# Kernel optimization log

Measured on AMD Instinct MI355X. Metric: run time of the kernel, lower is better.

The kernel has to match this reference:

```python
import jax, jax.numpy as jnp
import numpy as np

N_NODES = 100000   # multiple of 20 (tile factor)
N_BASE = N_NODES // 20
N_EDGES = 3200000  # avg degree 32


def setup_inputs() -> dict:
    key = jax.random.key(0)
    ks = jax.random.split(key, 12)
    x1 = jax.random.normal(ks[0], (N_NODES, 15), dtype=jnp.float32)
    x2 = jax.random.normal(ks[1], (N_BASE, 4), dtype=jnp.float32)
    edges = jax.random.randint(ks[2], (2, N_EDGES), 0, N_NODES, dtype=jnp.int64)
    # params (PyTorch Linear convention: y = x @ W.T + b)
    W1 = jax.random.normal(ks[3], (15, 15), dtype=jnp.float32) * 0.1
    b1 = jax.random.normal(ks[4], (15,), dtype=jnp.float32) * 0.1
    Wg = jax.random.normal(ks[5], (15, 34), dtype=jnp.float32) * 0.1  # GCNConv weight
    bg = jax.random.normal(ks[6], (15,), dtype=jnp.float32) * 0.1
    W3 = jax.random.normal(ks[7], (1, 34), dtype=jnp.float32) * 0.1
    b3 = jax.random.normal(ks[8], (1,), dtype=jnp.float32) * 0.1
    W4 = jax.random.normal(ks[9], (19, 19), dtype=jnp.float32) * 0.1
    b4 = jax.random.normal(ks[10], (19,), dtype=jnp.float32) * 0.1
    return {"x1": x1, "x2": x2, "edges": edges, "W1": W1, "b1": b1,
            "Wg": Wg, "bg": bg, "W3": W3, "b3": b3, "W4": W4, "b4": b4}


def reference(x1, x2, edges, W1, b1, Wg, bg, W3, b3, W4, b4):
    N = x1.shape[0]
    # b = layer4(cat([x1, tile(x2, (20,1))]))
    x2t = jnp.tile(x2, (20, 1))                       # [N, 4]
    b = jnp.concatenate([x1, x2t], axis=1) @ W4.T + b4  # [N, 19]
    a = jax.nn.relu(x1 @ W1.T + b1)                     # [N, 15]

    # GCN normalization with self-loops (PyG GCNConv defaults)
    row = jnp.concatenate([edges[0], jnp.arange(N, dtype=edges.dtype)])
    col = jnp.concatenate([edges[1], jnp.arange(N, dtype=edges.dtype)])
    deg = jax.ops.segment_sum(jnp.ones_like(col, dtype=x1.dtype), col, num_segments=N)
    dinv = jnp.where(deg > 0, deg ** -0.5, 0.0)
    norm = dinv[row] * dinv[col]                       # [E+N]

    for _ in range(5):
        h = jnp.concatenate([a, b], axis=1) @ Wg.T     # [N, 15]
        agg = jax.ops.segment_sum(h[row] * norm[:, None], col, num_segments=N)
        a = jax.nn.relu(agg + bg)

    out = jnp.concatenate([a, b], axis=1) @ W3.T + b3  # [N, 1]
    return jnp.tanh(out.mean())
```

## Files before the change

kernel.cpp:

```cpp
#include <hip/hip_runtime.h>
#include <hip/hip_fp16.h>
#include <math.h>

#define N_NODES 100000
#define N_BASE  5000
#define N_EDGES 3200000
#define NBKT    391
#define CAPB    9472
#define EPB     4096
#define GEB     782

__device__ inline unsigned pkh(float a, float b) {
    return (unsigned)__half_as_ushort(__float2half_rn(a)) |
           ((unsigned)__half_as_ushort(__float2half_rn(b)) << 16);
}

__device__ inline unsigned hadd2u(unsigned a, unsigned b) {
    __half2 r = __hadd2(*(__half2*)&a, *(__half2*)&b);
    return *(unsigned*)&r;
}

__global__ __launch_bounds__(512) void k_initg(int* __restrict__ gcur, float* __restrict__ bins) {
    int t = threadIdx.x;
    if (t < NBKT) gcur[t] = t * CAPB;
    if (t < 64) bins[t] = 0.0f;
}

__global__ __launch_bounds__(512) void k_bucket(const int* __restrict__ row, const int* __restrict__ col,
                                                int* __restrict__ gcur, unsigned* __restrict__ csr) {
    __shared__ int hist[NBKT], gbase[NBKT], curi[NBKT], excl[NBKT];
    __shared__ int sc[512];
    __shared__ unsigned sdst[EPB];
    __shared__ int sadr[EPB];
    int t = threadIdx.x;
    int e0 = blockIdx.x * EPB;
    int cnt = (N_EDGES - e0 < EPB) ? (N_EDGES - e0) : EPB;
    for (int k = t; k < NBKT; k += 512) hist[k] = 0;
    __syncthreads();
    for (int j = t; j < cnt; j += 512) atomicAdd(&hist[col[e0 + j] >> 8], 1);
    __syncthreads();
    sc[t] = (t < NBKT) ? hist[t] : 0;
    __syncthreads();
    for (int off = 1; off < 512; off <<= 1) {
        int v = (t >= off) ? sc[t - off] : 0;
        __syncthreads();
        sc[t] += v;
        __syncthreads();
    }
    if (t < NBKT) {
        int e = sc[t] - hist[t];
        excl[t] = e;
        curi[t] = e;
        gbase[t] = (hist[t] > 0) ? atomicAdd(&gcur[t], hist[t]) : 0;
    }
    __syncthreads();
    for (int j = t; j < cnt; j += 512) {
        int d = col[e0 + j];
        int s = row[e0 + j];
        int b = d >> 8;
        int pos = atomicAdd(&curi[b], 1);
        sdst[pos] = ((unsigned)(d & 255) << 17) | (unsigned)s;
        sadr[pos] = gbase[b] + (pos - excl[b]);
    }
    __syncthreads();
    for (int j = t; j < cnt; j += 512) csr[sadr[j]] = sdst[j];
}

__global__ __launch_bounds__(1024) void k_sort(const int* __restrict__ gcur, unsigned* __restrict__ csr,
                                               int* __restrict__ rs, int* __restrict__ re,
                                               float* __restrict__ dinv) {
    __shared__ unsigned stage[CAPB];
    __shared__ int hist[256], offs[256], cur[256];
    int t = threadIdx.x, b = blockIdx.x;
    int base = b * CAPB;
    int cnt = gcur[b] - base;
    if (t < 256) hist[t] = 0;
    for (int j = t; j < cnt; j += 1024) stage[j] = csr[base + j];
    __syncthreads();
    for (int j = t; j < cnt; j += 1024) atomicAdd(&hist[stage[j] >> 17], 1);
    __syncthreads();
    if (t < 256) offs[t] = hist[t];
    __syncthreads();
    for (int off = 1; off < 256; off <<= 1) {
        int v = 0;
        if (t < 256 && t >= off) v = offs[t - off];
        __syncthreads();
        if (t < 256) offs[t] += v;
        __syncthreads();
    }
    if (t < 256) {
        int excl = offs[t] - hist[t];
        cur[t] = excl;
        int node = b * 256 + t;
        if (node < N_NODES) {
            rs[node] = base + excl;
            re[node] = base + excl + hist[t];
            dinv[node] = rsqrtf((float)(hist[t] + 1));
        }
    }
    __syncthreads();
    for (int j = t; j < cnt; j += 1024) {
        unsigned p = stage[j];
        int slot = atomicAdd(&cur[p >> 17], 1);
        csr[base + slot] = p & 0x1FFFFu;
    }
}

__global__ __launch_bounds__(256) void k_ab_h(const float* __restrict__ x1, const float* __restrict__ x2,
                                              const float* __restrict__ W1, const float* __restrict__ b1,
                                              const float* __restrict__ W4, const float* __restrict__ b4,
                                              const float* __restrict__ Wg, const float* __restrict__ W3,
                                              const float* __restrict__ dinv,
                                              float* __restrict__ bb, __half* __restrict__ h0,
                                              float* __restrict__ bins) {
    __shared__ float sW1[225], sb1[15], sW4[361], sb4[19], sWg[510], sW3b[19];
    for (int t = threadIdx.x; t < 225; t += 256) sW1[t] = W1[t];
    for (int t = threadIdx.x; t < 361; t += 256) sW4[t] = W4[t];
    for (int t = threadIdx.x; t < 510; t += 256) sWg[t] = Wg[t];
    if (threadIdx.x < 15) sb1[threadIdx.x] = b1[threadIdx.x];
    if (threadIdx.x < 19) { sb4[threadIdx.x] = b4[threadIdx.x]; sW3b[threadIdx.x] = W3[15 + threadIdx.x]; }
    __syncthreads();
    int i = blockIdx.x * 256 + threadIdx.x;
    bool valid = i < N_NODES;
    int ii = valid ? i : 0;
    float x[15];
#pragma unroll
    for (int k = 0; k < 15; k++) x[k] = x1[(size_t)ii * 15 + k];
    float xt[4];
    int ib = ii % N_BASE;
#pragma unroll
    for (int k = 0; k < 4; k++) xt[k] = x2[(size_t)ib * 4 + k];
    float in[34];
    float bp = 0.0f;
#pragma unroll
    for (int o = 0; o < 19; o++) {
        float s = sb4[o];
#pragma unroll
        for (int k = 0; k < 15; k++) s += x[k] * sW4[o * 19 + k];
#pragma unroll
        for (int k = 0; k < 4; k++) s += xt[k] * sW4[o * 19 + 15 + k];
        in[15 + o] = s;
        bp += s * sW3b[o];
    }
#pragma unroll
    for (int o = 0; o < 15; o++) {
        float s = sb1[o];
#pragma unroll
        for (int k = 0; k < 15; k++) s += x[k] * sW1[o * 15 + k];
        in[o] = fmaxf(s, 0.0f);
    }
    float dn = dinv[ii];
    if (valid) {
        float4* bbp = (float4*)(bb + (size_t)ii * 20);
        bbp[0] = make_float4(in[15], in[16], in[17], in[18]);
        bbp[1] = make_float4(in[19], in[20], in[21], in[22]);
        bbp[2] = make_float4(in[23], in[24], in[25], in[26]);
        bbp[3] = make_float4(in[27], in[28], in[29], in[30]);
        bbp[4] = make_float4(in[31], in[32], in[33], 0.0f);
        float hv[15];
#pragma unroll
        for (int o = 0; o < 15; o++) {
            float s = 0.0f;
#pragma unroll
            for (int k = 0; k < 34; k++) s += in[k] * sWg[o * 34 + k];
            hv[o] = s * dn;
        }
        unsigned hu[8];
#pragma unroll
        for (int k = 0; k < 7; k++) hu[k] = pkh(hv[2 * k], hv[2 * k + 1]);
        hu[7] = pkh(hv[14], 0.0f);
        uint4* hp = (uint4*)(h0 + (size_t)ii * 16);
        hp[0] = make_uint4(hu[0], hu[1], hu[2], hu[3]);
        hp[1] = make_uint4(hu[4], hu[5], hu[6], hu[7]);
    }
    float val = valid ? bp : 0.0f;
#pragma unroll
    for (int off = 32; off > 0; off >>= 1) val += __shfl_down(val, off, 64);
    __shared__ float wsum[4];
    if ((threadIdx.x & 63) == 0) wsum[threadIdx.x >> 6] = val;
    __syncthreads();
    if (threadIdx.x == 0) atomicAdd(&bins[blockIdx.x & 63], wsum[0] + wsum[1] + wsum[2] + wsum[3]);
}

__global__ __launch_bounds__(1024) void k_gather(const int* __restrict__ rs, const int* __restrict__ re,
                                                 const unsigned* __restrict__ csr,
                                                 const __half* __restrict__ h_in,
                                                 const float* __restrict__ dinv,
                                                 const float* __restrict__ bb,
                                                 const float* __restrict__ Wg,
                                                 const float* __restrict__ bg,
                                                 const float* __restrict__ W3,
                                                 __half* __restrict__ h_out,
                                                 float* __restrict__ bins, int last) {
    __shared__ float sWg[544], sbg[16], sW3[16];
    __shared__ float ws2[16];
    int t = threadIdx.x;
    for (int k = t; k < 544; k += 1024) sWg[k] = (k < 510) ? Wg[k] : 0.0f;
    if (t < 16) { sbg[t] = (t < 15) ? bg[t] : 0.0f; sW3[t] = (t < 15) ? W3[t] : 0.0f; }
    __syncthreads();
    int wid = t >> 6;
    int n0 = blockIdx.x * 32 + wid * 2;
    int n1 = n0 + 1;
    int lane = t & 63, es = lane >> 1, half = lane & 1;
    int rs0 = rs[n0], deg0 = re[n0] - rs0;
    int rs1 = rs[n1], deg1 = re[n1] - rs1;
    const uint4* hp4 = (const uint4*)h_in;
    uint4 s0v = make_uint4(0u, 0u, 0u, 0u), s1v = make_uint4(0u, 0u, 0u, 0u);
    if (es == 0) s0v = hp4[(size_t)n0 * 2 + half];
    if (es == 1) s1v = hp4[(size_t)n1 * 2 + half];
    unsigned a00 = s0v.x, a01 = s0v.y, a02 = s0v.z, a03 = s0v.w;
    unsigned a10 = s1v.x, a11 = s1v.y, a12 = s1v.z, a13 = s1v.w;
    int degm = deg0 > deg1 ? deg0 : deg1;
    for (int base = 0; base < degm; base += 32) {
        int le = lane & 31;
        bool hi = lane >= 32;
        int src = hi ? rs1 : rs0;
        int dg = hi ? deg1 : deg0;
        unsigned ce = 0;
        if (base + le < dg) ce = csr[src + base + le];
        int lim0 = deg0 - base;
        int lim1 = deg1 - base;
        unsigned pa = __shfl(ce, es, 64);
        unsigned pb = __shfl(ce, 32 + es, 64);
        uint4 va = make_uint4(0u, 0u, 0u, 0u);
        uint4 vb = make_uint4(0u, 0u, 0u, 0u);
        if (es < lim0) va = hp4[(size_t)pa * 2 + half];
        if (es < lim1) vb = hp4[(size_t)pb * 2 + half];
        a00 = hadd2u(a00, va.x); a01 = hadd2u(a01, va.y);
        a02 = hadd2u(a02, va.z); a03 = hadd2u(a03, va.w);
        a10 = hadd2u(a10, vb.x); a11 = hadd2u(a11, vb.y);
        a12 = hadd2u(a12, vb.z); a13 = hadd2u(a13, vb.w);
    }
    int sel2 = (lane >> 1) & 1;
    int sel4 = (lane >> 2) & 1;
    unsigned kk0, kk1;
    {
        unsigned sA = sel2 ? a00 : a02, sB = sel2 ? a01 : a03;
        unsigned kA = sel2 ? a02 : a00, kB = sel2 ? a03 : a01;
        kA = hadd2u(kA, __shfl_xor(sA, 2, 64));
        kB = hadd2u(kB, __shfl_xor(sB, 2, 64));
        unsigned sd = sel4 ? kA : kB, kc = sel4 ? kB : kA;
        kc = hadd2u(kc, __shfl_xor(sd, 4, 64));
        kc = hadd2u(kc, __shfl_xor(kc, 8, 64));
        kc = hadd2u(kc, __shfl_xor(kc, 16, 64));
        kc = hadd2u(kc, __shfl_xor(kc, 32, 64));
        kk0 = kc;
    }
    {
        unsigned sA = sel2 ? a10 : a12, sB = sel2 ? a11 : a13;
        unsigned kA = sel2 ? a12 : a10, kB = sel2 ? a13 : a11;
        kA = hadd2u(kA, __shfl_xor(sA, 2, 64));
        kB = hadd2u(kB, __shfl_xor(sB, 2, 64));
        unsigned sd = sel4 ? kA : kB, kc = sel4 ? kB : kA;
        kc = hadd2u(kc, __shfl_xor(sd, 4, 64));
        kc = hadd2u(kc, __shfl_xor(kc, 8, 64));
        kc = hadd2u(kc, __shfl_xor(kc, 16, 64));
        kc = hadd2u(kc, __shfl_xor(kc, 32, 64));
        kk1 = kc;
    }
    int pr = 4 * half + 2 * sel2 + sel4;
    float dn0 = dinv[n0], dn1 = dinv[n1];
    float2 f0 = __half22float2(*(__half2*)&kk0);
    float2 f1 = __half22float2(*(__half2*)&kk1);
    float avx0 = fmaxf(dn0 * f0.x + sbg[2 * pr], 0.0f);
    float avy0 = fmaxf(dn0 * f0.y + sbg[2 * pr + 1], 0.0f);
    float avx1 = fmaxf(dn1 * f1.x + sbg[2 * pr], 0.0f);
    float avy1 = fmaxf(dn1 * f1.y + sbg[2 * pr + 1], 0.0f);
    if (!last) {
        int p = lane >> 3, c2e = lane & 7, o0 = 2 * c2e;
        int j0 = p >> 1, j1 = (p + 8) >> 1;
        int l0 = ((j0 & 1) << 2) | (j0 & 2) | ((j0 >> 2) & 1);
        int l1 = ((j1 & 1) << 2) | (j1 & 2) | ((j1 >> 2) & 1);
        float ex0a = __shfl(avx0, l0, 64), ey0a = __shfl(avy0, l0, 64);
        float ex1a = __shfl(avx0, l1, 64), ey1a = __shfl(avy0, l1, 64);
        float ex0b = __shfl(avx1, l0, 64), ey0b = __shfl(avy1, l0, 64);
        float ex1b = __shfl(avx1, l1, 64), ey1b = __shfl(avy1, l1, 64);
        float inv0a = (p & 1) ? ey0a : ex0a;
        float inv1a = (p & 1) ? ey1a : ex1a;
        float inv0b = (p & 1) ? ey0b : ex0b;
        float inv1b = (p & 1) ? ey1b : ex1b;
        if (p == 7) { inv1a = bb[(size_t)n0 * 20 + 0]; inv1b = bb[(size_t)n1 * 20 + 0]; }
        float wq0 = sWg[o0 * 34 + p],       wq1 = sWg[o0 * 34 + p + 8];
        float wr0 = sWg[(o0 + 1) * 34 + p], wr1 = sWg[(o0 + 1) * 34 + p + 8];
        float s0a = inv0a * wq0 + inv1a * wq1;
        float s1a = inv0a * wr0 + inv1a * wr1;
        float s0b = inv0b * wq0 + inv1b * wq1;
        float s1b = inv0b * wr0 + inv1b * wr1;
#pragma unroll
        for (int i = 2; i < 5; i++) {
            int k = p + 8 * i;
            if (k < 34) {
                float ia = bb[(size_t)n0 * 20 + (k - 15)];
                float ib2 = bb[(size_t)n1 * 20 + (k - 15)];
                float w0 = sWg[o0 * 34 + k], w1 = sWg[(o0 + 1) * 34 + k];
                s0a += ia * w0; s1a += ia * w1;
                s0b += ib2 * w0; s1b += ib2 * w1;
            }
        }
        s0a += __shfl_xor(s0a, 8, 64);  s1a += __shfl_xor(s1a, 8, 64);
        s0a += __shfl_xor(s0a, 16, 64); s1a += __shfl_xor(s1a, 16, 64);
        s0a += __shfl_xor(s0a, 32, 64); s1a += __shfl_xor(s1a, 32, 64);
        s0b += __shfl_xor(s0b, 8, 64);  s1b += __shfl_xor(s1b, 8, 64);
        s0b += __shfl_xor(s0b, 16, 64); s1b += __shfl_xor(s1b, 16, 64);
        s0b += __shfl_xor(s0b, 32, 64); s1b += __shfl_xor(s1b, 32, 64);
        if (p == 0) {
            ((unsigned*)h_out)[(size_t)n0 * 8 + c2e] = pkh(s0a * dn0, s1a * dn0);
            ((unsigned*)h_out)[(size_t)n1 * 8 + c2e] = pkh(s0b * dn1, s1b * dn1);
        }
    } else {
        float c = 0.0f;
        if (lane < 8) {
            c = avx0 * sW3[2 * pr] + avy0 * sW3[2 * pr + 1]
              + avx1 * sW3[2 * pr] + avy1 * sW3[2 * pr + 1];
        }
        c += __shfl_xor(c, 1, 64);
        c += __shfl_xor(c, 2, 64);
        c += __shfl_xor(c, 4, 64);
        if (lane == 0) ws2[wid] = c;
        __syncthreads();
        if (t == 0) {
            float s = 0.0f;
#pragma unroll
            for (int k = 0; k < 16; k++) s += ws2[k];
            atomicAdd(&bins[blockIdx.x & 63], s);
        }
    }
}

__global__ void k_finalize(const float* __restrict__ bins, const float* __restrict__ b3,
                           float* __restrict__ out) {
    float s = 0.0f;
    for (int k = 0; k < 64; k++) s += bins[k];
    out[0] = tanhf(s * (1.0f / (float)N_NODES) + b3[0]);
}

extern "C" void kernel_launch(void* const* d_in, const int* in_sizes, int n_in,
                              void* d_out, int out_size, void* d_ws, size_t ws_size,
                              hipStream_t stream) {
    const float* x1 = (const float*)d_in[0];
    const float* x2 = (const float*)d_in[1];
    const int* edges = (const int*)d_in[2];
    const float* W1 = (const float*)d_in[3];
    const float* b1 = (const float*)d_in[4];
    const float* Wg = (const float*)d_in[5];
    const float* bg = (const float*)d_in[6];
    const float* W3 = (const float*)d_in[7];
    const float* b3 = (const float*)d_in[8];
    const float* W4 = (const float*)d_in[9];
    const float* b4 = (const float*)d_in[10];

    const int* row = edges;
    const int* col = edges + N_EDGES;

    char* ws = (char*)d_ws;
    unsigned* csr  = (unsigned*)ws;
    float*    bb   = (float*)(csr + (size_t)NBKT * CAPB);
    __half*   h0   = (__half*)(bb + (size_t)N_NODES * 20);
    __half*   h1   = h0 + (size_t)N_NODES * 16;
    float*    dinv = (float*)(h1 + (size_t)N_NODES * 16);
    int*      rs   = (int*)(dinv + N_NODES);
    int*      re   = rs + N_NODES;
    int*      gcur = re + N_NODES;
    float*    bins = (float*)(gcur + NBKT);

    int gN = (N_NODES + 255) / 256;

    k_initg<<<1, 512, 0, stream>>>(gcur, bins);
    k_bucket<<<GEB, 512, 0, stream>>>(row, col, gcur, csr);
    k_sort<<<NBKT, 1024, 0, stream>>>(gcur, csr, rs, re, dinv);
    k_ab_h<<<gN, 256, 0, stream>>>(x1, x2, W1, b1, W4, b4, Wg, W3, dinv, bb, h0, bins);
    for (int t = 0; t < 5; t++) {
        const __half* hi = (t & 1) ? h1 : h0;
        __half* ho = (t & 1) ? h0 : h1;
        k_gather<<<N_NODES / 32, 1024, 0, stream>>>(rs, re, csr, hi, dinv, bb, Wg, bg, W3,
                                                    ho, bins, t == 4 ? 1 : 0);
    }
    k_finalize<<<1, 1, 0, stream>>>(bins, b3, (float*)d_out);
}
```

Measured before the change: 351.6 us.

## Remap gather so each half-wave owns one node and each lane loads full rows

```diff
diff --git a/kernel.cpp b/kernel.cpp
--- a/kernel.cpp
+++ b/kernel.cpp
@@ -200,81 +200,68 @@
     __syncthreads();
     int wid = t >> 6;
     int n0 = blockIdx.x * 32 + wid * 2;
-    int n1 = n0 + 1;
-    int lane = t & 63, es = lane >> 1, half = lane & 1;
-    int rs0 = rs[n0], deg0 = re[n0] - rs0;
-    int rs1 = rs[n1], deg1 = re[n1] - rs1;
+    int lane = t & 63, g = lane >> 5, lg = lane & 31;
+    int ng = n0 + g;
+    int rsg = rs[ng];
+    int degg = re[ng] - rsg;
+    int dego = __shfl_xor(degg, 32, 64);
+    int degm = degg > dego ? degg : dego;
     const uint4* hp4 = (const uint4*)h_in;
-    uint4 s0v = make_uint4(0u, 0u, 0u, 0u), s1v = make_uint4(0u, 0u, 0u, 0u);
-    if (es == 0) s0v = hp4[(size_t)n0 * 2 + half];
-    if (es == 1) s1v = hp4[(size_t)n1 * 2 + half];
-    unsigned a00 = s0v.x, a01 = s0v.y, a02 = s0v.z, a03 = s0v.w;
-    unsigned a10 = s1v.x, a11 = s1v.y, a12 = s1v.z, a13 = s1v.w;
-    int degm = deg0 > deg1 ? deg0 : deg1;
-    for (int base = 0; base < degm; base += 32) {
-        int le = lane & 31;
-        bool hi = lane >= 32;
-        int src = hi ? rs1 : rs0;
-        int dg = hi ? deg1 : deg0;
-        unsigned ce = 0;
-        if (base + le < dg) ce = csr[src + base + le];
-        int lim0 = deg0 - base;
-        int lim1 = deg1 - base;
-        unsigned pa = __shfl(ce, es, 64);
-        unsigned pb = __shfl(ce, 32 + es, 64);
-        uint4 va = make_uint4(0u, 0u, 0u, 0u);
-        uint4 vb = make_uint4(0u, 0u, 0u, 0u);
-        if (es < lim0) va = hp4[(size_t)pa * 2 + half];
-        if (es < lim1) vb = hp4[(size_t)pb * 2 + half];
-        a00 = hadd2u(a00, va.x); a01 = hadd2u(a01, va.y);
-        a02 = hadd2u(a02, va.z); a03 = hadd2u(a03, va.w);
-        a10 = hadd2u(a10, vb.x); a11 = hadd2u(a11, vb.y);
-        a12 = hadd2u(a12, vb.z); a13 = hadd2u(a13, vb.w);
-    }
-    int sel2 = (lane >> 1) & 1;
-    int sel4 = (lane >> 2) & 1;
-    unsigned kk0, kk1;
-    {
-        unsigned sA = sel2 ? a00 : a02, sB = sel2 ? a01 : a03;
-        unsigned kA = sel2 ? a02 : a00, kB = sel2 ? a03 : a01;
-        kA = hadd2u(kA, __shfl_xor(sA, 2, 64));
-        kB = hadd2u(kB, __shfl_xor(sB, 2, 64));
-        unsigned sd = sel4 ? kA : kB, kc = sel4 ? kB : kA;
-        kc = hadd2u(kc, __shfl_xor(sd, 4, 64));
-        kc = hadd2u(kc, __shfl_xor(kc, 8, 64));
-        kc = hadd2u(kc, __shfl_xor(kc, 16, 64));
-        kc = hadd2u(kc, __shfl_xor(kc, 32, 64));
-        kk0 = kc;
-    }
-    {
-        unsigned sA = sel2 ? a10 : a12, sB = sel2 ? a11 : a13;
-        unsigned kA = sel2 ? a12 : a10, kB = sel2 ? a13 : a11;
-        kA = hadd2u(kA, __shfl_xor(sA, 2, 64));
-        kB = hadd2u(kB, __shfl_xor(sB, 2, 64));
-        unsigned sd = sel4 ? kA : kB, kc = sel4 ? kB : kA;
-        kc = hadd2u(kc, __shfl_xor(sd, 4, 64));
-        kc = hadd2u(kc, __shfl_xor(kc, 8, 64));
-        kc = hadd2u(kc, __shfl_xor(kc, 16, 64));
-        kc = hadd2u(kc, __shfl_xor(kc, 32, 64));
-        kk1 = kc;
-    }
-    int pr = 4 * half + 2 * sel2 + sel4;
-    float dn0 = dinv[n0], dn1 = dinv[n1];
-    float2 f0 = __half22float2(*(__half2*)&kk0);
-    float2 f1 = __half22float2(*(__half2*)&kk1);
-    float avx0 = fmaxf(dn0 * f0.x + sbg[2 * pr], 0.0f);
-    float avy0 = fmaxf(dn0 * f0.y + sbg[2 * pr + 1], 0.0f);
-    float avx1 = fmaxf(dn1 * f1.x + sbg[2 * pr], 0.0f);
-    float avy1 = fmaxf(dn1 * f1.y + sbg[2 * pr + 1], 0.0f);
+    uint4 sL = make_uint4(0u, 0u, 0u, 0u), sH = make_uint4(0u, 0u, 0u, 0u);
+    if (lg == 0) { sL = hp4[(size_t)ng * 2]; sH = hp4[(size_t)ng * 2 + 1]; }
+    unsigned a0 = sL.x, a1 = sL.y, a2 = sL.z, a3 = sL.w;
+    unsigned a4 = sH.x, a5 = sH.y, a6 = sH.z, a7 = sH.w;
+    for (int base = 0; base < degm; base += 64) {
+        bool vA = base + lg < degg;
+        bool vB = base + 32 + lg < degg;
+        unsigned pa = 0u, pb = 0u;
+        if (vA) pa = csr[rsg + base + lg];
+        if (vB) pb = csr[rsg + base + 32 + lg];
+        uint4 vaL = make_uint4(0u, 0u, 0u, 0u), vaH = make_uint4(0u, 0u, 0u, 0u);
+        uint4 vbL = make_uint4(0u, 0u, 0u, 0u), vbH = make_uint4(0u, 0u, 0u, 0u);
+        if (vA) { vaL = hp4[(size_t)pa * 2]; vaH = hp4[(size_t)pa * 2 + 1]; }
+        if (vB) { vbL = hp4[(size_t)pb * 2]; vbH = hp4[(size_t)pb * 2 + 1]; }
+        a0 = hadd2u(a0, vaL.x); a1 = hadd2u(a1, vaL.y);
+        a2 = hadd2u(a2, vaL.z); a3 = hadd2u(a3, vaL.w);
+        a4 = hadd2u(a4, vaH.x); a5 = hadd2u(a5, vaH.y);
+        a6 = hadd2u(a6, vaH.z); a7 = hadd2u(a7, vaH.w);
+        a0 = hadd2u(a0, vbL.x); a1 = hadd2u(a1, vbL.y);
+        a2 = hadd2u(a2, vbL.z); a3 = hadd2u(a3, vbL.w);
+        a4 = hadd2u(a4, vbH.x); a5 = hadd2u(a5, vbH.y);
+        a6 = hadd2u(a6, vbH.z); a7 = hadd2u(a7, vbH.w);
+    }
+    int b0 = lg & 1, b1 = (lg >> 1) & 1, b2 = (lg >> 2) & 1;
+    unsigned kA0 = b0 ? a4 : a0, kA1 = b0 ? a5 : a1, kA2 = b0 ? a6 : a2, kA3 = b0 ? a7 : a3;
+    unsigned sA0 = b0 ? a0 : a4, sA1 = b0 ? a1 : a5, sA2 = b0 ? a2 : a6, sA3 = b0 ? a3 : a7;
+    kA0 = hadd2u(kA0, __shfl_xor(sA0, 1, 64));
+    kA1 = hadd2u(kA1, __shfl_xor(sA1, 1, 64));
+    kA2 = hadd2u(kA2, __shfl_xor(sA2, 1, 64));
+    kA3 = hadd2u(kA3, __shfl_xor(sA3, 1, 64));
+    unsigned kB0 = b1 ? kA2 : kA0, kB1 = b1 ? kA3 : kA1;
+    unsigned sB0 = b1 ? kA0 : kA2, sB1 = b1 ? kA1 : kA3;
+    kB0 = hadd2u(kB0, __shfl_xor(sB0, 2, 64));
+    kB1 = hadd2u(kB1, __shfl_xor(sB1, 2, 64));
+    unsigned kk = b2 ? kB1 : kB0;
+    unsigned sd = b2 ? kB0 : kB1;
+    kk = hadd2u(kk, __shfl_xor(sd, 4, 64));
+    kk = hadd2u(kk, __shfl_xor(kk, 8, 64));
+    kk = hadd2u(kk, __shfl_xor(kk, 16, 64));
+    int pr = 4 * b0 + 2 * b1 + b2;
+    float dng = dinv[ng];
+    float2 f = __half22float2(*(__half2*)&kk);
+    float avx = fmaxf(dng * f.x + sbg[2 * pr], 0.0f);
+    float avy = fmaxf(dng * f.y + sbg[2 * pr + 1], 0.0f);
     if (!last) {
+        int n1 = n0 + 1;
+        float dn0 = __shfl(dng, 0, 64), dn1 = __shfl(dng, 32, 64);
         int p = lane >> 3, c2e = lane & 7, o0 = 2 * c2e;
         int j0 = p >> 1, j1 = (p + 8) >> 1;
         int l0 = ((j0 & 1) << 2) | (j0 & 2) | ((j0 >> 2) & 1);
         int l1 = ((j1 & 1) << 2) | (j1 & 2) | ((j1 >> 2) & 1);
-        float ex0a = __shfl(avx0, l0, 64), ey0a = __shfl(avy0, l0, 64);
-        float ex1a = __shfl(avx0, l1, 64), ey1a = __shfl(avy0, l1, 64);
-        float ex0b = __shfl(avx1, l0, 64), ey0b = __shfl(avy1, l0, 64);
-        float ex1b = __shfl(avx1, l1, 64), ey1b = __shfl(avy1, l1, 64);
+        float ex0a = __shfl(avx, l0, 64),      ey0a = __shfl(avy, l0, 64);
+        float ex1a = __shfl(avx, l1, 64),      ey1a = __shfl(avy, l1, 64);
+        float ex0b = __shfl(avx, 32 + l0, 64), ey0b = __shfl(avy, 32 + l0, 64);
+        float ex1b = __shfl(avx, 32 + l1, 64), ey1b = __shfl(avy, 32 + l1, 64);
         float inv0a = (p & 1) ? ey0a : ex0a;
         float inv1a = (p & 1) ? ey1a : ex1a;
         float inv0b = (p & 1) ? ey0b : ex0b;
@@ -309,13 +296,11 @@
         }
     } else {
         float c = 0.0f;
-        if (lane < 8) {
-            c = avx0 * sW3[2 * pr] + avy0 * sW3[2 * pr + 1]
-              + avx1 * sW3[2 * pr] + avy1 * sW3[2 * pr + 1];
-        }
+        if (lg < 8) c = avx * sW3[2 * pr] + avy * sW3[2 * pr + 1];
         c += __shfl_xor(c, 1, 64);
         c += __shfl_xor(c, 2, 64);
         c += __shfl_xor(c, 4, 64);
+        c += __shfl_xor(c, 32, 64);
         if (lane == 0) ws2[wid] = c;
         __syncthreads();
         if (t == 0) {
```

Result: no change. 344.8 us (-1.9%).
